# Kernel tuning notes

Measured on AMD Instinct MI355X. Metric: run time of the kernel, lower is better.

The kernel has to match this reference:

```python
import jax, jax.numpy as jnp
import numpy as np

B, SEQ, DIM, D, K = 32, 2048, 512, 512, 128


def _ln(x, g, b, eps=1e-5):
    m = x.mean(-1, keepdims=True)
    v = ((x - m) ** 2).mean(-1, keepdims=True)
    return (x - m) / jnp.sqrt(v + eps) * g + b


def _gelu(v):
    return jax.nn.gelu(v, approximate=False)


def _diff_topk(s, k, t):
    # s: (B, N) scores; iterative relaxed top-k (Xie & Ermon style).
    def step(carry, _):
        a = jax.nn.softmax(carry / t, axis=-1)
        carry = carry + jnp.log(jnp.clip(1.0 - a, 1e-6, 1.0))
        return carry, a
    _, Ws = jax.lax.scan(step, s, None, length=k)  # (k, B, N)
    return jnp.transpose(Ws, (1, 0, 2))            # (B, k, N)


def setup_inputs():
    key = jax.random.key(0)
    ks = jax.random.split(key, 6)
    w = lambda k_, shape: jax.random.normal(k_, shape, dtype=jnp.float32) * 0.02
    return {
        'x': jax.random.normal(ks[0], (B, SEQ, DIM), dtype=jnp.float32),
        'tau': jnp.array(0.0, dtype=jnp.float32),
        'ln1_g': jnp.ones((DIM,), jnp.float32), 'ln1_b': jnp.zeros((DIM,), jnp.float32),
        'W1': w(ks[1], (DIM, D)), 'b1': jnp.zeros((D,), jnp.float32),
        'ln2_g': jnp.ones((SEQ,), jnp.float32), 'ln2_b': jnp.zeros((SEQ,), jnp.float32),
        'W2': w(ks[2], (SEQ, SEQ)), 'b2': jnp.zeros((SEQ,), jnp.float32),
        'ln3_g': jnp.ones((D,), jnp.float32), 'ln3_b': jnp.zeros((D,), jnp.float32),
        'W3': w(ks[3], (D, D + 1)), 'b3': jnp.zeros((D + 1,), jnp.float32),
        'ln4_g': jnp.ones((D,), jnp.float32), 'ln4_b': jnp.zeros((D,), jnp.float32),
        'W4': w(ks[4], (D, DIM)), 'b4': jnp.zeros((DIM,), jnp.float32),
    }


def reference(x, tau, ln1_g, ln1_b, W1, b1, ln2_g, ln2_b, W2, b2,
              ln3_g, ln3_b, W3, b3, ln4_g, ln4_b, W4, b4):
    # tok_proj: LN(dim) -> Linear(dim, D) -> GELU
    x_tok = _gelu(_ln(x, ln1_g, ln1_b) @ W1 + b1)                  # (B, N, D)
    # ch_proj over the token axis: LN(seq) -> Linear(seq, seq) -> GELU
    xt = jnp.swapaxes(x_tok, 1, 2)                                  # (B, D, N)
    x_ch = jnp.swapaxes(_gelu(_ln(xt, ln2_g, ln2_b) @ W2 + b2), 1, 2)
    # proj -> split score | features
    h = _ln(x_tok + x_ch, ln3_g, ln3_b) @ W3 + b3                   # (B, N, D+1)
    x_score, x_proj = h[..., 0], h[..., 1:]
    t = jax.nn.sigmoid(jnp.clip(tau, -2.0, 5.0))
    Wmat = _diff_topk(x_score, K, t)                                # (B, k, N)
    Z = jnp.einsum('bkn,bnd->bkd', Wmat, x_proj)                    # soft gather
    Y = jnp.einsum('bkn,bkd->bnd', Wmat, Z)                         # soft scatter
    return _ln(x_proj + Y, ln4_g, ln4_b) @ W4 + b4                  # (B, N, dim)
```

## Files before the change

### kernel.cpp

```cpp
#include <hip/hip_runtime.h>
#include <math.h>

#define B_   32
#define SEQ_ 2048
#define DIM_ 512
#define KSEL 128

typedef _Float16 f16;
typedef _Float16 half8 __attribute__((ext_vector_type(8)));
typedef float floatx4 __attribute__((ext_vector_type(4)));

#define LSTR2 32

__device__ __forceinline__ float gelu_exact(float v) {
  return 0.5f * v * (1.0f + erff(v * 0.70710678118654752440f));
}

__global__ __launch_bounds__(256) void rowstats512(const float* __restrict__ X,
                                                   float* __restrict__ mean,
                                                   float* __restrict__ rstd) {
  int row = blockIdx.x * 4 + (threadIdx.x >> 6);
  int l = threadIdx.x & 63;
  const float4* p = (const float4*)(X + (size_t)row * 512);
  float4 v0 = p[l * 2], v1 = p[l * 2 + 1];
  float s = v0.x + v0.y + v0.z + v0.w + v1.x + v1.y + v1.z + v1.w;
  float q = v0.x*v0.x + v0.y*v0.y + v0.z*v0.z + v0.w*v0.w
          + v1.x*v1.x + v1.y*v1.y + v1.z*v1.z + v1.w*v1.w;
#pragma unroll
  for (int off = 32; off > 0; off >>= 1) {
    s += __shfl_down(s, off);
    q += __shfl_down(q, off);
  }
  if (l == 0) {
    float m = s * (1.0f / 512.0f);
    float var = q * (1.0f / 512.0f) - m * m;
    mean[row] = m;
    rstd[row] = rsqrtf(var + 1e-5f);
  }
}

__global__ __launch_bounds__(256) void rowstats512_f16(const f16* __restrict__ X,
                                                       float* __restrict__ mean,
                                                       float* __restrict__ rstd) {
  int row = blockIdx.x * 4 + (threadIdx.x >> 6);
  int l = threadIdx.x & 63;
  half8 h = *(const half8*)(X + (size_t)row * 512 + l * 8);
  float s = 0.f, q = 0.f;
#pragma unroll
  for (int i = 0; i < 8; ++i) { float v = (float)h[i]; s += v; q += v * v; }
#pragma unroll
  for (int off = 32; off > 0; off >>= 1) {
    s += __shfl_down(s, off);
    q += __shfl_down(q, off);
  }
  if (l == 0) {
    float m = s * (1.0f / 512.0f);
    float var = q * (1.0f / 512.0f) - m * m;
    mean[row] = m;
    rstd[row] = rsqrtf(var + 1e-5f);
  }
}

__global__ __launch_bounds__(512) void colstats_part(const f16* __restrict__ xtok,
                                                     float2* __restrict__ part) {
  int b = blockIdx.x >> 3, pr = blockIdx.x & 7;
  int d = threadIdx.x;
  const f16* src = xtok + ((size_t)b * SEQ_ + (size_t)pr * 256) * 512 + d;
  float s = 0.f, q = 0.f;
#pragma unroll 4
  for (int i = 0; i < 256; ++i) {
    float v = (float)src[(size_t)i * 512];
    s += v; q += v * v;
  }
  part[(size_t)blockIdx.x * 512 + d] = make_float2(s, q);
}

__global__ __launch_bounds__(256) void colstats_fin(const float2* __restrict__ part,
                                                    float* __restrict__ mean,
                                                    float* __restrict__ rstd) {
  int idx = blockIdx.x * 256 + threadIdx.x;
  int b = idx >> 9;
  float s = 0.f, q = 0.f;
#pragma unroll
  for (int p = 0; p < 8; ++p) {
    float2 v = part[((size_t)(b * 8 + p)) * 512 + (idx & 511)];
    s += v.x; q += v.y;
  }
  float m = s * (1.0f / 2048.0f);
  mean[idx] = m;
  rstd[idx] = rsqrtf(q * (1.0f / 2048.0f) - m * m + 1e-5f);
}

template <typename T>
__global__ __launch_bounds__(256) void transpose_cvt(const T* __restrict__ src,
                                                     f16* __restrict__ dst,
                                                     int R, int C, long sb, long db) {
  __shared__ float tile[32][33];
  const T* s = src + (long)blockIdx.z * sb;
  f16* d = dst + (long)blockIdx.z * db;
  int c0 = blockIdx.x * 32, r0 = blockIdx.y * 32;
  int tx = threadIdx.x, ty = threadIdx.y;
#pragma unroll
  for (int i = 0; i < 4; ++i) {
    int r = r0 + ty + i * 8, c = c0 + tx;
    if (r < R && c < C) tile[ty + i * 8][tx] = (float)s[(long)r * C + c];
  }
  __syncthreads();
#pragma unroll
  for (int i = 0; i < 4; ++i) {
    int c = c0 + ty + i * 8, r = r0 + tx;
    if (c < C && r < R) d[(long)c * R + r] = (f16)tile[tx][ty + i * 8];
  }
}

__global__ __launch_bounds__(256) void trans2_kernel(const f16* __restrict__ xtok,
    const float* __restrict__ mean2, const float* __restrict__ rstd2,
    const float* __restrict__ g2, const float* __restrict__ bl2,
    f16* __restrict__ A2) {
  __shared__ float tile[32][33];
  int b = blockIdx.z;
  const f16* src = xtok + (long)b * SEQ_ * 512;
  f16* dst = A2 + (long)b * 512 * SEQ_;
  int d0 = blockIdx.x * 32, s0 = blockIdx.y * 32;
  int tx = threadIdx.x, ty = threadIdx.y;
  float m = mean2[b * 512 + d0 + tx];
  float rs = rstd2[b * 512 + d0 + tx];
#pragma unroll
  for (int i = 0; i < 4; ++i) {
    int s = s0 + ty + i * 8;
    float v = (float)src[(long)s * 512 + d0 + tx];
    tile[ty + i * 8][tx] = (v - m) * rs * g2[s] + bl2[s];
  }
  __syncthreads();
#pragma unroll
  for (int i = 0; i < 4; ++i) {
    int d = d0 + ty + i * 8, s = s0 + tx;
    dst[(long)d * SEQ_ + s] = (f16)tile[tx][ty + i * 8];
  }
}


__device__ __forceinline__ void stage_gll(const f16* __restrict__ src, long ld,
                                          int row0, int k0, f16* S, int t) {
  int w = t >> 6, lane = t & 63;
  int r = lane >> 2, c8 = (lane & 3) * 8;
#pragma unroll
  for (int i = 0; i < 2; ++i) {
    int chunk = w * 2 + i;
    const f16* g = src + (long)(row0 + chunk * 16 + r) * ld + k0 + c8;
    f16* l = S + chunk * 16 * LSTR2;
    __builtin_amdgcn_global_load_lds(
        (const __attribute__((address_space(1))) void*)g,
        (__attribute__((address_space(3))) void*)l, 16, 0, 0);
  }
}

__device__ __forceinline__ void stage_a_ln_f32(const float* __restrict__ src, long ld,
    const float* __restrict__ mean, const float* __restrict__ rstd,
    const float* __restrict__ g, const float* __restrict__ bl,
    int row0, int k0, f16* S, int t) {
  int row = t >> 1, kc = (t & 1) * 16;
  int r = row0 + row, c = k0 + kc;
  float m = mean[r], sd = rstd[r];
  const float* p = src + (long)r * ld + c;
  float v[16], gv[16], bv[16];
#pragma unroll
  for (int i = 0; i < 4; ++i) {
    float4 q = ((const float4*)p)[i];
    v[i*4+0]=q.x; v[i*4+1]=q.y; v[i*4+2]=q.z; v[i*4+3]=q.w;
    float4 gq = ((const float4*)(g + c))[i];
    gv[i*4+0]=gq.x; gv[i*4+1]=gq.y; gv[i*4+2]=gq.z; gv[i*4+3]=gq.w;
    float4 bq = ((const float4*)(bl + c))[i];
    bv[i*4+0]=bq.x; bv[i*4+1]=bq.y; bv[i*4+2]=bq.z; bv[i*4+3]=bq.w;
  }
  half8 o0, o1;
#pragma unroll
  for (int i = 0; i < 8; ++i) {
    o0[i] = (f16)((v[i] - m) * sd * gv[i] + bv[i]);
    o1[i] = (f16)((v[i + 8] - m) * sd * gv[i + 8] + bv[i + 8]);
  }
  *(half8*)(S + row * LSTR2 + kc) = o0;
  *(half8*)(S + row * LSTR2 + kc + 8) = o1;
}

__device__ __forceinline__ void stage_a_ln_f16(const f16* __restrict__ src, long ld,
    const float* __restrict__ mean, const float* __restrict__ rstd,
    const float* __restrict__ g, const float* __restrict__ bl,
    int row0, int k0, f16* S, int t) {
  int row = t >> 1, kc = (t & 1) * 16;
  int r = row0 + row, c = k0 + kc;
  float m = mean[r], sd = rstd[r];
  const f16* p = src + (long)r * ld + c;
  half8 h0 = *(const half8*)(p);
  half8 h1 = *(const half8*)(p + 8);
  float gv[16], bv[16];
#pragma unroll
  for (int i = 0; i < 4; ++i) {
    float4 gq = ((const float4*)(g + c))[i];
    gv[i*4+0]=gq.x; gv[i*4+1]=gq.y; gv[i*4+2]=gq.z; gv[i*4+3]=gq.w;
    float4 bq = ((const float4*)(bl + c))[i];
    bv[i*4+0]=bq.x; bv[i*4+1]=bq.y; bv[i*4+2]=bq.z; bv[i*4+3]=bq.w;
  }
  half8 o0, o1;
#pragma unroll
  for (int i = 0; i < 8; ++i) {
    o0[i] = (f16)(((float)h0[i] - m) * sd * gv[i] + bv[i]);
    o1[i] = (f16)(((float)h1[i] - m) * sd * gv[i + 8] + bv[i + 8]);
  }
  *(half8*)(S + row * LSTR2 + kc) = o0;
  *(half8*)(S + row * LSTR2 + kc + 8) = o1;
}

__device__ __forceinline__ void mfma_step(const f16* As, const f16* Bs, int lane,
                                          int wr, int wc, floatx4 acc[4][4]) {
  int kc = (lane >> 4) * 8;
  int rl = lane & 15;
  half8 a[4], b[4];
#pragma unroll
  for (int mi = 0; mi < 4; ++mi)
    a[mi] = *(const half8*)(As + (wr * 64 + mi * 16 + rl) * LSTR2 + kc);
#pragma unroll
  for (int ni = 0; ni < 4; ++ni)
    b[ni] = *(const half8*)(Bs + (wc * 64 + ni * 16 + rl) * LSTR2 + kc);
#pragma unroll
  for (int mi = 0; mi < 4; ++mi)
#pragma unroll
    for (int ni = 0; ni < 4; ++ni)
      acc[mi][ni] = __builtin_amdgcn_mfma_f32_16x16x32_f16(a[mi], b[ni], acc[mi][ni], 0, 0, 0);
}

#define GEMM_PROLOG \
  __shared__ __attribute__((aligned(16))) f16 As[128 * LSTR2]; \
  __shared__ __attribute__((aligned(16))) f16 Bs[128 * LSTR2]; \
  int t = threadIdx.x; \
  int lane = t & 63, w = t >> 6, wr = w >> 1, wc = w & 1; \
  floatx4 acc[4][4]; \
  _Pragma("unroll") for (int mi = 0; mi < 4; ++mi) \
  _Pragma("unroll") for (int ni = 0; ni < 4; ++ni) acc[mi][ni] = (floatx4){0.f,0.f,0.f,0.f};

__global__ __launch_bounds__(256) void g1_kernel(const float* __restrict__ x,
    const float* __restrict__ mean, const float* __restrict__ rstd,
    const float* __restrict__ g1, const float* __restrict__ bl1,
    const f16* __restrict__ W1T, const float* __restrict__ b1,
    f16* __restrict__ xtok) {
  GEMM_PROLOG
  int m0 = blockIdx.y * 128, n0 = blockIdx.x * 128;
  for (int k0 = 0; k0 < 512; k0 += 32) {
    stage_a_ln_f32(x, 512, mean, rstd, g1, bl1, m0, k0, As, t);
    stage_gll(W1T, 512, n0, k0, Bs, t);
    __syncthreads();
    mfma_step(As, Bs, lane, wr, wc, acc);
    __syncthreads();
  }
#pragma unroll
  for (int mi = 0; mi < 4; ++mi)
#pragma unroll
    for (int ni = 0; ni < 4; ++ni) {
      int c = n0 + wc * 64 + ni * 16 + (lane & 15);
      float bias = b1[c];
      int r0 = m0 + wr * 64 + mi * 16 + (lane >> 4) * 4;
#pragma unroll
      for (int j = 0; j < 4; ++j)
        xtok[(long)(r0 + j) * 512 + c] = (f16)gelu_exact(acc[mi][ni][j] + bias);
    }
}

__global__ __launch_bounds__(256) void g2_kernel(const f16* __restrict__ W2T,
    const f16* __restrict__ A2, const float* __restrict__ b2,
    const f16* __restrict__ xtok, f16* __restrict__ xsum) {
  GEMM_PROLOG
  int b = blockIdx.z;
  int m0 = blockIdx.y * 128, n0 = blockIdx.x * 128;
  const f16* A2b = A2 + (long)b * 512 * SEQ_;
  const f16* xtb = xtok + (long)b * SEQ_ * 512;
  f16* xsb = xsum + (long)b * SEQ_ * 512;
  for (int k0 = 0; k0 < SEQ_; k0 += 32) {
    stage_gll(W2T, SEQ_, m0, k0, As, t);
    stage_gll(A2b, SEQ_, n0, k0, Bs, t);
    __syncthreads();
    mfma_step(As, Bs, lane, wr, wc, acc);
    __syncthreads();
  }
#pragma unroll
  for (int mi = 0; mi < 4; ++mi)
#pragma unroll
    for (int ni = 0; ni < 4; ++ni) {
      int c = n0 + wc * 64 + ni * 16 + (lane & 15);
      int r0 = m0 + wr * 64 + mi * 16 + (lane >> 4) * 4;
#pragma unroll
      for (int j = 0; j < 4; ++j) {
        int r = r0 + j;
        long idx = (long)r * 512 + c;
        float v = gelu_exact(acc[mi][ni][j] + b2[r]);
        xsb[idx] = (f16)((float)xtb[idx] + v);
      }
    }
}

__global__ __launch_bounds__(256) void g3_kernel(const f16* __restrict__ xsum,
    const float* __restrict__ mean, const float* __restrict__ rstd,
    const float* __restrict__ g3, const float* __restrict__ bl3,
    const f16* __restrict__ BT , const float* __restrict__ b3,
    f16* __restrict__ xproj) {
  GEMM_PROLOG
  int m0 = blockIdx.y * 128, n0 = blockIdx.x * 128;
  for (int k0 = 0; k0 < 512; k0 += 32) {
    stage_a_ln_f16(xsum, 512, mean, rstd, g3, bl3, m0, k0, As, t);
    stage_gll(BT, 512, n0, k0, Bs, t);
    __syncthreads();
    mfma_step(As, Bs, lane, wr, wc, acc);
    __syncthreads();
  }
#pragma unroll
  for (int mi = 0; mi < 4; ++mi)
#pragma unroll
    for (int ni = 0; ni < 4; ++ni) {
      int c = n0 + wc * 64 + ni * 16 + (lane & 15);
      float bias = b3[c + 1];
      int r0 = m0 + wr * 64 + mi * 16 + (lane >> 4) * 4;
#pragma unroll
      for (int j = 0; j < 4; ++j)
        xproj[(long)(r0 + j) * 512 + c] = (f16)(acc[mi][ni][j] + bias);
    }
}

__global__ __launch_bounds__(256) void score_kernel(const f16* __restrict__ xsum,
    const float* __restrict__ mean, const float* __restrict__ rstd,
    const float* __restrict__ g3, const float* __restrict__ bl3,
    const f16* __restrict__ w3c , const float* __restrict__ b3,
    float* __restrict__ xscore) {
  int row = blockIdx.x * 4 + (threadIdx.x >> 6);
  int l = threadIdx.x & 63;
  float m = mean[row], sd = rstd[row];
  half8 h = *(const half8*)(xsum + (long)row * 512 + l * 8);
  half8 wv = *(const half8*)(w3c + l * 8);
  float acc = 0.f;
#pragma unroll
  for (int i = 0; i < 8; ++i) {
    int d = l * 8 + i;
    float v = ((float)h[i] - m) * sd * g3[d] + bl3[d];
    acc += v * (float)wv[i];
  }
#pragma unroll
  for (int off = 32; off > 0; off >>= 1) acc += __shfl_down(acc, off);
  if (l == 0) xscore[row] = acc + b3[0];
}

__global__ __launch_bounds__(256) void topk_kernel(const float* __restrict__ xscore,
                                                   const float* __restrict__ tau,
                                                   f16* __restrict__ Wm) {
  int b = blockIdx.x, t = threadIdx.x;
  __shared__ float red[4];
  float tv = fminf(fmaxf(tau[0], -2.0f), 5.0f);
  float temp = 1.0f / (1.0f + expf(-tv));
  float it = 1.0f / temp;
  float c[8];
  const float* xs = xscore + (size_t)b * SEQ_;
#pragma unroll
  for (int i = 0; i < 8; ++i) c[i] = xs[t * 8 + i];
  for (int k = 0; k < KSEL; ++k) {
    float e[8];
    float p = 0.f;
#pragma unroll
    for (int i = 0; i < 8; ++i) { e[i] = expf(c[i] * it); p += e[i]; }
#pragma unroll
    for (int off = 32; off > 0; off >>= 1) p += __shfl_down(p, off);
    if ((t & 63) == 0) red[t >> 6] = p;
    __syncthreads();
    float S = red[0] + red[1] + red[2] + red[3];
    float iS = 1.0f / S;
    float a[8];
    half8 h;
#pragma unroll
    for (int i = 0; i < 8; ++i) { a[i] = e[i] * iS; h[i] = (f16)a[i]; }
    *(half8*)(Wm + ((size_t)b * KSEL + k) * SEQ_ + t * 8) = h;
#pragma unroll
    for (int i = 0; i < 8; ++i) c[i] += logf(fmaxf(1.0f - a[i], 1e-6f));
    __syncthreads();
  }
}

__global__ __launch_bounds__(256) void gz_kernel(const f16* __restrict__ Wm,
    const f16* __restrict__ xprojT, float* __restrict__ Zpart) {
  GEMM_PROLOG
  int b = blockIdx.z, kc = blockIdx.y;
  int n0 = blockIdx.x * 128;
  const f16* A = Wm + (long)b * KSEL * SEQ_;
  const f16* BT = xprojT + (long)b * 512 * SEQ_;
  float* Zb = Zpart + ((long)b * 2 + kc) * KSEL * 512;
  int kbeg = kc * 1024, kend = kbeg + 1024;
  for (int k0 = kbeg; k0 < kend; k0 += 32) {
    stage_gll(A, SEQ_, 0, k0, As, t);
    stage_gll(BT, SEQ_, n0, k0, Bs, t);
    __syncthreads();
    mfma_step(As, Bs, lane, wr, wc, acc);
    __syncthreads();
  }
#pragma unroll
  for (int mi = 0; mi < 4; ++mi)
#pragma unroll
    for (int ni = 0; ni < 4; ++ni) {
      int c = n0 + wc * 64 + ni * 16 + (lane & 15);
      int r0 = wr * 64 + mi * 16 + (lane >> 4) * 4;
#pragma unroll
      for (int j = 0; j < 4; ++j)
        Zb[(long)(r0 + j) * 512 + c] = acc[mi][ni][j];
    }
}

__global__ __launch_bounds__(256) void ztrans_kernel(const float* __restrict__ Zpart,
                                                     f16* __restrict__ ZT) {
  __shared__ float tile[32][33];
  int b = blockIdx.z;
  int c0 = blockIdx.x * 32, r0 = blockIdx.y * 32;
  int tx = threadIdx.x, ty = threadIdx.y;
  const float* p0 = Zpart + ((long)b * 2 + 0) * KSEL * 512;
  const float* p1 = Zpart + ((long)b * 2 + 1) * KSEL * 512;
#pragma unroll
  for (int i = 0; i < 4; ++i) {
    int r = r0 + ty + i * 8, c = c0 + tx;
    tile[ty + i * 8][tx] = p0[(long)r * 512 + c] + p1[(long)r * 512 + c];
  }
  __syncthreads();
  f16* d = ZT + (long)b * 512 * KSEL;
#pragma unroll
  for (int i = 0; i < 4; ++i) {
    int c = c0 + ty + i * 8, r = r0 + tx;
    d[(long)c * KSEL + r] = (f16)tile[tx][ty + i * 8];
  }
}

__global__ __launch_bounds__(256) void gy_kernel(const f16* __restrict__ WmT,
    const f16* __restrict__ ZT, const f16* __restrict__ xproj,
    f16* __restrict__ rbuf) {
  GEMM_PROLOG
  int b = blockIdx.z;
  int m0 = blockIdx.y * 128, n0 = blockIdx.x * 128;
  const f16* A = WmT + (long)b * SEQ_ * KSEL;
  const f16* BT = ZT + (long)b * 512 * KSEL;
  const f16* xpb = xproj + (long)b * SEQ_ * 512;
  f16* rb = rbuf + (long)b * SEQ_ * 512;
  for (int k0 = 0; k0 < KSEL; k0 += 32) {
    stage_gll(A, KSEL, m0, k0, As, t);
    stage_gll(BT, KSEL, n0, k0, Bs, t);
    __syncthreads();
    mfma_step(As, Bs, lane, wr, wc, acc);
    __syncthreads();
  }
#pragma unroll
  for (int mi = 0; mi < 4; ++mi)
#pragma unroll
    for (int ni = 0; ni < 4; ++ni) {
      int c = n0 + wc * 64 + ni * 16 + (lane & 15);
      int r0 = m0 + wr * 64 + mi * 16 + (lane >> 4) * 4;
#pragma unroll
      for (int j = 0; j < 4; ++j) {
        long idx = (long)(r0 + j) * 512 + c;
        rb[idx] = (f16)((float)xpb[idx] + acc[mi][ni][j]);
      }
    }
}

__global__ __launch_bounds__(256) void g4_kernel(const f16* __restrict__ rbuf,
    const float* __restrict__ mean, const float* __restrict__ rstd,
    const float* __restrict__ g4, const float* __restrict__ bl4,
    const f16* __restrict__ W4T, const float* __restrict__ b4,
    float* __restrict__ out) {
  GEMM_PROLOG
  int m0 = blockIdx.y * 128, n0 = blockIdx.x * 128;
  for (int k0 = 0; k0 < 512; k0 += 32) {
    stage_a_ln_f16(rbuf, 512, mean, rstd, g4, bl4, m0, k0, As, t);
    stage_gll(W4T, 512, n0, k0, Bs, t);
    __syncthreads();
    mfma_step(As, Bs, lane, wr, wc, acc);
    __syncthreads();
  }
#pragma unroll
  for (int mi = 0; mi < 4; ++mi)
#pragma unroll
    for (int ni = 0; ni < 4; ++ni) {
      int c = n0 + wc * 64 + ni * 16 + (lane & 15);
      float bias = b4[c];
      int r0 = m0 + wr * 64 + mi * 16 + (lane >> 4) * 4;
#pragma unroll
      for (int j = 0; j < 4; ++j)
        out[(long)(r0 + j) * 512 + c] = acc[mi][ni][j] + bias;
    }
}

extern "C" void kernel_launch(void* const* d_in, const int* in_sizes, int n_in,
                              void* d_out, int out_size, void* d_ws, size_t ws_size,
                              hipStream_t stream) {
  const float* x    = (const float*)d_in[0];
  const float* tau  = (const float*)d_in[1];
  const float* g1   = (const float*)d_in[2];
  const float* bl1  = (const float*)d_in[3];
  const float* W1   = (const float*)d_in[4];
  const float* b1   = (const float*)d_in[5];
  const float* g2   = (const float*)d_in[6];
  const float* bl2  = (const float*)d_in[7];
  const float* W2   = (const float*)d_in[8];
  const float* b2   = (const float*)d_in[9];
  const float* g3   = (const float*)d_in[10];
  const float* bl3  = (const float*)d_in[11];
  const float* W3   = (const float*)d_in[12];
  const float* b3   = (const float*)d_in[13];
  const float* g4   = (const float*)d_in[14];
  const float* bl4  = (const float*)d_in[15];
  const float* W4   = (const float*)d_in[16];
  const float* b4   = (const float*)d_in[17];
  float* out = (float*)d_out;

  const long NTOK = (long)B_ * SEQ_;

  char* ws = (char*)d_ws;
  f16* regA   = (f16*)(ws);
  f16* regB   = (f16*)(ws + (64l << 20));
  float* Zpart = (float*)(ws + (128l << 20));
  f16* W2T    = (f16*)(ws + (144l << 20));
  f16* W1T    = (f16*)(ws + (152l << 20));
  f16* W3T    = (f16*)(ws + (153l << 20));
  f16* W4T    = (f16*)(ws + (154l << 20));
  float* xscore = (float*)(ws + (155l << 20));
  float* meanA  = (float*)(ws + (156l << 20));
  float* rstdA  = meanA + NTOK;
  float* mean2  = rstdA + NTOK;
  float* rstd2  = mean2 + B_ * 512;
  float2* part  = (float2*)(rstd2 + B_ * 512);

  f16* xtok   = (f16*)d_out;
  f16* xprojT = (f16*)d_out;
  f16* Wm     = (f16*)((char*)d_out + (64l << 20));
  f16* WmT    = (f16*)((char*)d_out + (80l << 20));
  f16* ZT     = (f16*)((char*)d_out + (96l << 20));

  f16* A2    = regA;
  f16* xsum  = regB;
  f16* xproj = regA;
  f16* rbuf  = regB;

  dim3 tb(32, 8);

  transpose_cvt<float><<<dim3(16, 16, 1), tb, 0, stream>>>(W1, W1T, 512, 512, 0, 0);
  transpose_cvt<float><<<dim3(64, 64, 1), tb, 0, stream>>>(W2, W2T, 2048, 2048, 0, 0);
  transpose_cvt<float><<<dim3(17, 16, 1), tb, 0, stream>>>(W3, W3T, 512, 513, 0, 0);
  transpose_cvt<float><<<dim3(16, 16, 1), tb, 0, stream>>>(W4, W4T, 512, 512, 0, 0);

  rowstats512<<<NTOK / 4, 256, 0, stream>>>(x, meanA, rstdA);
  g1_kernel<<<dim3(4, 512), 256, 0, stream>>>(x, meanA, rstdA, g1, bl1, W1T, b1, xtok);

  colstats_part<<<B_ * 8, 512, 0, stream>>>(xtok, part);
  colstats_fin<<<64, 256, 0, stream>>>(part, mean2, rstd2);
  trans2_kernel<<<dim3(16, 64, B_), tb, 0, stream>>>(xtok, mean2, rstd2, g2, bl2, A2);
  g2_kernel<<<dim3(4, 16, B_), 256, 0, stream>>>(W2T, A2, b2, xtok, xsum);

  rowstats512_f16<<<NTOK / 4, 256, 0, stream>>>(xsum, meanA, rstdA);
  score_kernel<<<NTOK / 4, 256, 0, stream>>>(xsum, meanA, rstdA, g3, bl3, W3T, b3, xscore);
  g3_kernel<<<dim3(4, 512), 256, 0, stream>>>(xsum, meanA, rstdA, g3, bl3, W3T + 512, b3, xproj);

  topk_kernel<<<B_, 256, 0, stream>>>(xscore, tau, Wm);

  transpose_cvt<f16><<<dim3(16, 64, B_), tb, 0, stream>>>(xproj, xprojT, 2048, 512,
      (long)SEQ_ * 512, (long)512 * SEQ_);
  transpose_cvt<f16><<<dim3(64, 4, B_), tb, 0, stream>>>(Wm, WmT, 128, 2048,
      (long)KSEL * SEQ_, (long)SEQ_ * KSEL);

  gz_kernel<<<dim3(4, 2, B_), 256, 0, stream>>>(Wm, xprojT, Zpart);
  ztrans_kernel<<<dim3(16, 4, B_), tb, 0, stream>>>(Zpart, ZT);

  gy_kernel<<<dim3(4, 16, B_), 256, 0, stream>>>(WmT, ZT, xproj, rbuf);

  rowstats512_f16<<<NTOK / 4, 256, 0, stream>>>(rbuf, meanA, rstdA);
  g4_kernel<<<dim3(4, 512), 256, 0, stream>>>(rbuf, meanA, rstdA, g4, bl4, W4T, b4, out);
}
```

Baseline: 878.3 us.

## Narrow GEMM tiles, fuse xproj transpose into g3, widen topk block

The g2 and gz GEMMs move to 128x64 output tiles, and gz gets a 4-way split over the reduction axis, so more blocks are in flight. The g3 epilogue now also writes the transposed xprojT directly, which removes a separate transpose kernel. topk runs 512 threads with double-buffered reduction slots, dropping one barrier per iteration. The costs are lower per-block operand reuse, more Zpart partial traffic, and scattered 8-byte transposed stores from g3.

```diff
diff --git a/kernel.cpp b/kernel.cpp
--- a/kernel.cpp
+++ b/kernel.cpp
@@ -8,6 +8,7 @@
 
 typedef _Float16 f16;
 typedef _Float16 half8 __attribute__((ext_vector_type(8)));
+typedef _Float16 half4 __attribute__((ext_vector_type(4)));
 typedef float floatx4 __attribute__((ext_vector_type(4)));
 
 #define LSTR2 32
@@ -139,7 +140,6 @@
   }
 }
 
-
 __device__ __forceinline__ void stage_gll(const f16* __restrict__ src, long ld,
                                           int row0, int k0, f16* S, int t) {
   int w = t >> 6, lane = t & 63;
@@ -153,6 +153,16 @@
         (const __attribute__((address_space(1))) void*)g,
         (__attribute__((address_space(3))) void*)l, 16, 0, 0);
   }
+}
+
+__device__ __forceinline__ void stage_gll64(const f16* __restrict__ src, long ld,
+                                            int k0, f16* S, int t) {
+  int row = t >> 2, c8 = (t & 3) * 8;
+  const f16* g = src + (long)row * ld + k0 + c8;
+  f16* l = S + (t >> 6) * 16 * LSTR2;
+  __builtin_amdgcn_global_load_lds(
+      (const __attribute__((address_space(1))) void*)g,
+      (__attribute__((address_space(3))) void*)l, 16, 0, 0);
 }
 
 __device__ __forceinline__ void stage_a_ln_f32(const float* __restrict__ src, long ld,
@@ -229,6 +239,24 @@
       acc[mi][ni] = __builtin_amdgcn_mfma_f32_16x16x32_f16(a[mi], b[ni], acc[mi][ni], 0, 0, 0);
 }
 
+__device__ __forceinline__ void mfma_step_n64(const f16* As, const f16* Bs, int lane,
+                                              int wr, int wc, floatx4 acc[4][2]) {
+  int kc = (lane >> 4) * 8;
+  int rl = lane & 15;
+  half8 a[4], b[2];
+#pragma unroll
+  for (int mi = 0; mi < 4; ++mi)
+    a[mi] = *(const half8*)(As + (wr * 64 + mi * 16 + rl) * LSTR2 + kc);
+#pragma unroll
+  for (int ni = 0; ni < 2; ++ni)
+    b[ni] = *(const half8*)(Bs + (wc * 32 + ni * 16 + rl) * LSTR2 + kc);
+#pragma unroll
+  for (int mi = 0; mi < 4; ++mi)
+#pragma unroll
+    for (int ni = 0; ni < 2; ++ni)
+      acc[mi][ni] = __builtin_amdgcn_mfma_f32_16x16x32_f16(a[mi], b[ni], acc[mi][ni], 0, 0, 0);
+}
+
 #define GEMM_PROLOG \
   __shared__ __attribute__((aligned(16))) f16 As[128 * LSTR2]; \
   __shared__ __attribute__((aligned(16))) f16 Bs[128 * LSTR2]; \
@@ -237,6 +265,16 @@
   floatx4 acc[4][4]; \
   _Pragma("unroll") for (int mi = 0; mi < 4; ++mi) \
   _Pragma("unroll") for (int ni = 0; ni < 4; ++ni) acc[mi][ni] = (floatx4){0.f,0.f,0.f,0.f};
+
+#define GEMM_PROLOG_N64 \
+  __shared__ __attribute__((aligned(16))) f16 As[128 * LSTR2]; \
+  __shared__ __attribute__((aligned(16))) f16 Bs[64 * LSTR2]; \
+  int t = threadIdx.x; \
+  int lane = t & 63, w = t >> 6, wr = w >> 1, wc = w & 1; \
+  int rl = lane & 15, sl = lane >> 4; \
+  floatx4 acc[4][2]; \
+  _Pragma("unroll") for (int mi = 0; mi < 4; ++mi) \
+  _Pragma("unroll") for (int ni = 0; ni < 2; ++ni) acc[mi][ni] = (floatx4){0.f,0.f,0.f,0.f};
 
 __global__ __launch_bounds__(256) void g1_kernel(const float* __restrict__ x,
     const float* __restrict__ mean, const float* __restrict__ rstd,
@@ -268,29 +306,30 @@
 __global__ __launch_bounds__(256) void g2_kernel(const f16* __restrict__ W2T,
     const f16* __restrict__ A2, const float* __restrict__ b2,
     const f16* __restrict__ xtok, f16* __restrict__ xsum) {
-  GEMM_PROLOG
+  GEMM_PROLOG_N64
   int b = blockIdx.z;
-  int m0 = blockIdx.y * 128, n0 = blockIdx.x * 128;
-  const f16* A2b = A2 + (long)b * 512 * SEQ_;
+  int m0 = blockIdx.y * 128, n0 = blockIdx.x * 64;
+  const f16* Am = W2T + (long)m0 * SEQ_;
+  const f16* Bm = A2 + (long)b * 512 * SEQ_ + (long)n0 * SEQ_;
   const f16* xtb = xtok + (long)b * SEQ_ * 512;
   f16* xsb = xsum + (long)b * SEQ_ * 512;
   for (int k0 = 0; k0 < SEQ_; k0 += 32) {
-    stage_gll(W2T, SEQ_, m0, k0, As, t);
-    stage_gll(A2b, SEQ_, n0, k0, Bs, t);
-    __syncthreads();
-    mfma_step(As, Bs, lane, wr, wc, acc);
-    __syncthreads();
-  }
-#pragma unroll
-  for (int mi = 0; mi < 4; ++mi)
-#pragma unroll
-    for (int ni = 0; ni < 4; ++ni) {
-      int c = n0 + wc * 64 + ni * 16 + (lane & 15);
-      int r0 = m0 + wr * 64 + mi * 16 + (lane >> 4) * 4;
+    stage_gll(Am, SEQ_, 0, k0, As, t);
+    stage_gll64(Bm, SEQ_, k0, Bs, t);
+    __syncthreads();
+    mfma_step_n64(As, Bs, lane, wr, wc, acc);
+    __syncthreads();
+  }
+#pragma unroll
+  for (int mi = 0; mi < 4; ++mi)
+#pragma unroll
+    for (int ni = 0; ni < 2; ++ni) {
+      int cc = n0 + wc * 32 + ni * 16 + rl;
+      int r0 = m0 + wr * 64 + mi * 16 + sl * 4;
 #pragma unroll
       for (int j = 0; j < 4; ++j) {
         int r = r0 + j;
-        long idx = (long)r * 512 + c;
+        long idx = (long)r * 512 + cc;
         float v = gelu_exact(acc[mi][ni][j] + b2[r]);
         xsb[idx] = (f16)((float)xtb[idx] + v);
       }
@@ -301,7 +340,7 @@
     const float* __restrict__ mean, const float* __restrict__ rstd,
     const float* __restrict__ g3, const float* __restrict__ bl3,
     const f16* __restrict__ BT , const float* __restrict__ b3,
-    f16* __restrict__ xproj) {
+    f16* __restrict__ xproj, f16* __restrict__ xprojT) {
   GEMM_PROLOG
   int m0 = blockIdx.y * 128, n0 = blockIdx.x * 128;
   for (int k0 = 0; k0 < 512; k0 += 32) {
@@ -318,16 +357,23 @@
       int c = n0 + wc * 64 + ni * 16 + (lane & 15);
       float bias = b3[c + 1];
       int r0 = m0 + wr * 64 + mi * 16 + (lane >> 4) * 4;
-#pragma unroll
-      for (int j = 0; j < 4; ++j)
-        xproj[(long)(r0 + j) * 512 + c] = (f16)(acc[mi][ni][j] + bias);
+      half4 xp;
+#pragma unroll
+      for (int j = 0; j < 4; ++j) {
+        f16 v = (f16)(acc[mi][ni][j] + bias);
+        xproj[(long)(r0 + j) * 512 + c] = v;
+        xp[j] = v;
+      }
+      long bb = r0 >> 11;
+      long rloc = r0 & 2047;
+      *(half4*)(xprojT + (bb * 512 + c) * SEQ_ + rloc) = xp;
     }
 }
 
 __global__ __launch_bounds__(256) void score_kernel(const f16* __restrict__ xsum,
     const float* __restrict__ mean, const float* __restrict__ rstd,
     const float* __restrict__ g3, const float* __restrict__ bl3,
-    const f16* __restrict__ w3c , const float* __restrict__ b3,
+    const f16* __restrict__ w3c, const float* __restrict__ b3,
     float* __restrict__ xscore) {
   int row = blockIdx.x * 4 + (threadIdx.x >> 6);
   int l = threadIdx.x & 63;
@@ -346,65 +392,69 @@
   if (l == 0) xscore[row] = acc + b3[0];
 }
 
-__global__ __launch_bounds__(256) void topk_kernel(const float* __restrict__ xscore,
+__global__ __launch_bounds__(512) void topk_kernel(const float* __restrict__ xscore,
                                                    const float* __restrict__ tau,
                                                    f16* __restrict__ Wm) {
   int b = blockIdx.x, t = threadIdx.x;
-  __shared__ float red[4];
+  __shared__ float red[2][8];
   float tv = fminf(fmaxf(tau[0], -2.0f), 5.0f);
   float temp = 1.0f / (1.0f + expf(-tv));
   float it = 1.0f / temp;
-  float c[8];
+  float c[4];
   const float* xs = xscore + (size_t)b * SEQ_;
-#pragma unroll
-  for (int i = 0; i < 8; ++i) c[i] = xs[t * 8 + i];
+  {
+    float4 v = *(const float4*)(xs + t * 4);
+    c[0] = v.x; c[1] = v.y; c[2] = v.z; c[3] = v.w;
+  }
+  int l = t & 63, wid = t >> 6;
   for (int k = 0; k < KSEL; ++k) {
-    float e[8];
+    float e[4];
     float p = 0.f;
 #pragma unroll
-    for (int i = 0; i < 8; ++i) { e[i] = expf(c[i] * it); p += e[i]; }
+    for (int i = 0; i < 4; ++i) { e[i] = expf(c[i] * it); p += e[i]; }
 #pragma unroll
     for (int off = 32; off > 0; off >>= 1) p += __shfl_down(p, off);
-    if ((t & 63) == 0) red[t >> 6] = p;
-    __syncthreads();
-    float S = red[0] + red[1] + red[2] + red[3];
+    if (l == 0) red[k & 1][wid] = p;
+    __syncthreads();
+    float S = 0.f;
+#pragma unroll
+    for (int q = 0; q < 8; ++q) S += red[k & 1][q];
     float iS = 1.0f / S;
-    float a[8];
-    half8 h;
-#pragma unroll
-    for (int i = 0; i < 8; ++i) { a[i] = e[i] * iS; h[i] = (f16)a[i]; }
-    *(half8*)(Wm + ((size_t)b * KSEL + k) * SEQ_ + t * 8) = h;
-#pragma unroll
-    for (int i = 0; i < 8; ++i) c[i] += logf(fmaxf(1.0f - a[i], 1e-6f));
-    __syncthreads();
+    half4 h;
+    float a[4];
+#pragma unroll
+    for (int i = 0; i < 4; ++i) { a[i] = e[i] * iS; h[i] = (f16)a[i]; }
+    *(half4*)(Wm + ((size_t)b * KSEL + k) * SEQ_ + t * 4) = h;
+#pragma unroll
+    for (int i = 0; i < 4; ++i) c[i] += logf(fmaxf(1.0f - a[i], 1e-6f));
   }
 }
 
 __global__ __launch_bounds__(256) void gz_kernel(const f16* __restrict__ Wm,
     const f16* __restrict__ xprojT, float* __restrict__ Zpart) {
-  GEMM_PROLOG
+  GEMM_PROLOG_N64
   int b = blockIdx.z, kc = blockIdx.y;
-  int n0 = blockIdx.x * 128;
-  const f16* A = Wm + (long)b * KSEL * SEQ_;
-  const f16* BT = xprojT + (long)b * 512 * SEQ_;
-  float* Zb = Zpart + ((long)b * 2 + kc) * KSEL * 512;
-  int kbeg = kc * 1024, kend = kbeg + 1024;
+  int n0 = blockIdx.x * 64;
+  const f16* Am = Wm + (long)b * KSEL * SEQ_;
+  const f16* Bm = xprojT + (long)b * 512 * SEQ_ + (long)n0 * SEQ_;
+  float* Zb = Zpart + ((long)b * 4 + kc) * KSEL * 512;
+  int kbeg = kc * 512, kend = kbeg + 512;
   for (int k0 = kbeg; k0 < kend; k0 += 32) {
-    stage_gll(A, SEQ_, 0, k0, As, t);
-    stage_gll(BT, SEQ_, n0, k0, Bs, t);
-    __syncthreads();
-    mfma_step(As, Bs, lane, wr, wc, acc);
-    __syncthreads();
-  }
-#pragma unroll
-  for (int mi = 0; mi < 4; ++mi)
-#pragma unroll
-    for (int ni = 0; ni < 4; ++ni) {
-      int c = n0 + wc * 64 + ni * 16 + (lane & 15);
-      int r0 = wr * 64 + mi * 16 + (lane >> 4) * 4;
+    stage_gll(Am, SEQ_, 0, k0, As, t);
+    stage_gll64(Bm, SEQ_, k0, Bs, t);
+    __syncthreads();
+    mfma_step_n64(As, Bs, lane, wr, wc, acc);
+    __syncthreads();
+  }
+#pragma unroll
+  for (int mi = 0; mi < 4; ++mi)
+#pragma unroll
+    for (int ni = 0; ni < 2; ++ni) {
+      int cc = n0 + wc * 32 + ni * 16 + rl;
+      int r0 = wr * 64 + mi * 16 + sl * 4;
 #pragma unroll
       for (int j = 0; j < 4; ++j)
-        Zb[(long)(r0 + j) * 512 + c] = acc[mi][ni][j];
+        Zb[(long)(r0 + j) * 512 + cc] = acc[mi][ni][j];
     }
 }
 
@@ -414,12 +464,15 @@
   int b = blockIdx.z;
   int c0 = blockIdx.x * 32, r0 = blockIdx.y * 32;
   int tx = threadIdx.x, ty = threadIdx.y;
-  const float* p0 = Zpart + ((long)b * 2 + 0) * KSEL * 512;
-  const float* p1 = Zpart + ((long)b * 2 + 1) * KSEL * 512;
+  const float* p0 = Zpart + ((long)b * 4 + 0) * KSEL * 512;
+  const float* p1 = Zpart + ((long)b * 4 + 1) * KSEL * 512;
+  const float* p2 = Zpart + ((long)b * 4 + 2) * KSEL * 512;
+  const float* p3 = Zpart + ((long)b * 4 + 3) * KSEL * 512;
 #pragma unroll
   for (int i = 0; i < 4; ++i) {
     int r = r0 + ty + i * 8, c = c0 + tx;
-    tile[ty + i * 8][tx] = p0[(long)r * 512 + c] + p1[(long)r * 512 + c];
+    long idx = (long)r * 512 + c;
+    tile[ty + i * 8][tx] = (p0[idx] + p1[idx]) + (p2[idx] + p3[idx]);
   }
   __syncthreads();
   f16* d = ZT + (long)b * 512 * KSEL;
@@ -516,7 +569,6 @@
   char* ws = (char*)d_ws;
   f16* regA   = (f16*)(ws);
   f16* regB   = (f16*)(ws + (64l << 20));
-  float* Zpart = (float*)(ws + (128l << 20));
   f16* W2T    = (f16*)(ws + (144l << 20));
   f16* W1T    = (f16*)(ws + (152l << 20));
   f16* W3T    = (f16*)(ws + (153l << 20));
@@ -527,12 +579,13 @@
   float* mean2  = rstdA + NTOK;
   float* rstd2  = mean2 + B_ * 512;
   float2* part  = (float2*)(rstd2 + B_ * 512);
+  f16* ZT     = (f16*)(ws + (157l << 20));
 
   f16* xtok   = (f16*)d_out;
   f16* xprojT = (f16*)d_out;
   f16* Wm     = (f16*)((char*)d_out + (64l << 20));
   f16* WmT    = (f16*)((char*)d_out + (80l << 20));
-  f16* ZT     = (f16*)((char*)d_out + (96l << 20));
+  float* Zpart = (float*)((char*)d_out + (96l << 20));
 
   f16* A2    = regA;
   f16* xsum  = regB;
@@ -552,20 +605,19 @@
   colstats_part<<<B_ * 8, 512, 0, stream>>>(xtok, part);
   colstats_fin<<<64, 256, 0, stream>>>(part, mean2, rstd2);
   trans2_kernel<<<dim3(16, 64, B_), tb, 0, stream>>>(xtok, mean2, rstd2, g2, bl2, A2);
-  g2_kernel<<<dim3(4, 16, B_), 256, 0, stream>>>(W2T, A2, b2, xtok, xsum);
+  g2_kernel<<<dim3(8, 16, B_), 256, 0, stream>>>(W2T, A2, b2, xtok, xsum);
 
   rowstats512_f16<<<NTOK / 4, 256, 0, stream>>>(xsum, meanA, rstdA);
   score_kernel<<<NTOK / 4, 256, 0, stream>>>(xsum, meanA, rstdA, g3, bl3, W3T, b3, xscore);
-  g3_kernel<<<dim3(4, 512), 256, 0, stream>>>(xsum, meanA, rstdA, g3, bl3, W3T + 512, b3, xproj);
-
-  topk_kernel<<<B_, 256, 0, stream>>>(xscore, tau, Wm);
-
-  transpose_cvt<f16><<<dim3(16, 64, B_), tb, 0, stream>>>(xproj, xprojT, 2048, 512,
-      (long)SEQ_ * 512, (long)512 * SEQ_);
+  g3_kernel<<<dim3(4, 512), 256, 0, stream>>>(xsum, meanA, rstdA, g3, bl3, W3T + 512, b3,
+                                              xproj, xprojT);
+
+  topk_kernel<<<B_, 512, 0, stream>>>(xscore, tau, Wm);
+
   transpose_cvt<f16><<<dim3(64, 4, B_), tb, 0, stream>>>(Wm, WmT, 128, 2048,
       (long)KSEL * SEQ_, (long)SEQ_ * KSEL);
 
-  gz_kernel<<<dim3(4, 2, B_), 256, 0, stream>>>(Wm, xprojT, Zpart);
+  gz_kernel<<<dim3(8, 4, B_), 256, 0, stream>>>(Wm, xprojT, Zpart);
   ztrans_kernel<<<dim3(16, 4, B_), tb, 0, stream>>>(Zpart, ZT);
 
   gy_kernel<<<dim3(4, 16, B_), 256, 0, stream>>>(WmT, ZT, xproj, rbuf);
```

After: 938.6 us. 6.9% more time.
